# Kernel tuning notes

Measured on AMD Instinct MI355X. Metric: run time of the kernel, lower is better.

Reference implementation:

```python
import jax, jax.numpy as jnp
import numpy as np

T, BATCH, DIM = 2048, 32, 512

def setup_inputs() -> dict:
    key = jax.random.key(0)
    ks = jax.random.split(key, 9)
    s = 1.0 / np.sqrt(DIM)
    return {
        "x": jax.random.normal(ks[0], (T, BATCH, DIM), dtype=jnp.float32),
        "W_in": jax.random.uniform(ks[1], (2 * DIM, DIM), jnp.float32, -s, s),
        "b_in": jax.random.uniform(ks[2], (2 * DIM,), jnp.float32, -s, s),
        "W_out": jax.random.uniform(ks[3], (DIM, DIM), jnp.float32, -s, s),
        "b_out": jax.random.uniform(ks[4], (DIM,), jnp.float32, -s, s),
        "A": jax.random.normal(ks[5], (DIM,), dtype=jnp.float32) * 0.1,
        "B": jax.random.normal(ks[6], (DIM,), dtype=jnp.float32) * 0.1,
        "gamma": jnp.ones((DIM,), dtype=jnp.float32),
        "beta": jnp.zeros((DIM,), dtype=jnp.float32),
    }

def _layernorm(y, gamma, beta, eps=1e-5):
    mu = jnp.mean(y, axis=-1, keepdims=True)
    var = jnp.mean(jnp.square(y - mu), axis=-1, keepdims=True)
    return (y - mu) * jax.lax.rsqrt(var + eps) * gamma + beta

def reference(x, W_in, b_in, W_out, b_out, A, B, gamma, beta):
    # in_proj then chunk along last dim: z first half, g second half
    zg = jnp.einsum('tbd,ed->tbe', x, W_in) + b_in          # [T,B,2D]
    z, g = jnp.split(zg, 2, axis=-1)
    g = jax.nn.sigmoid(g)
    Bz = B * z                                              # [T,B,D]
    gA = g * A                                              # [T,B,D]

    # diagonal linear recurrence h_t = gA_t * h_{t-1} + Bz_t
    def step(prev, inp):
        ga_t, bz_t = inp
        curr = ga_t * prev + bz_t
        return curr, curr

    h0 = jnp.zeros((x.shape[1], x.shape[2]), dtype=x.dtype)
    _, h = jax.lax.scan(step, h0, (gA, Bz))                 # [T,B,D]

    out = jnp.einsum('tbd,ed->tbe', h, W_out) + b_out
    return _layernorm(x + out, gamma, beta)
```

## Files before the change

kernel.cpp:

```cpp
#include <hip/hip_runtime.h>
#include <hip/hip_bf16.h>
#include <cstdint>
#include <cstddef>

#define T_LEN 2048
#define BATCH 32
#define DIM 512
#define M_TOT (T_LEN * BATCH)
#define K_DIM DIM
#define N1 (2 * DIM)
#define NCHUNK 64
#define CLEN (T_LEN / NCHUNK)
#define BD (BATCH * DIM)
#define MT_TILES (M_TOT / 128)

typedef unsigned short ushort_t;
typedef __attribute__((ext_vector_type(8))) short short8;
typedef __attribute__((ext_vector_type(4))) float floatx4;
typedef __attribute__((ext_vector_type(4))) unsigned short ushort4v;

__device__ __forceinline__ float bf2f(ushort_t u) {
  union { unsigned int i; float f; } v;
  v.i = ((unsigned int)u) << 16;
  return v.f;
}
__device__ __forceinline__ ushort_t f2bf(float f) {
  union { float f; unsigned int i; } v;
  v.f = f;
  unsigned int x = v.i;
  return (ushort_t)((x + 0x7fffu + ((x >> 16) & 1u)) >> 16);
}

__device__ __forceinline__ void async16(const void* gp, void* lp) {
  __builtin_amdgcn_global_load_lds(
      (__attribute__((address_space(1))) void*)(void*)gp,
      (__attribute__((address_space(3))) void*)lp, 16, 0, 0);
}

__global__ __launch_bounds__(256) void cvt_f32_bf16(const float* __restrict__ in,
                                                    ushort_t* __restrict__ out,
                                                    int n4) {
  int i = blockIdx.x * 256 + threadIdx.x;
  if (i >= n4) return;
  const floatx4 v = *((const floatx4*)in + i);
  ushort4v o;
  o.x = f2bf(v.x); o.y = f2bf(v.y); o.z = f2bf(v.z); o.w = f2bf(v.w);
  *((ushort4v*)out + i) = o;
}

__global__ __launch_bounds__(256, 2) void gemm_in(
    const ushort_t* __restrict__ Ag, const ushort_t* __restrict__ Bg,
    const float* __restrict__ bias, const float* __restrict__ Avec,
    const float* __restrict__ Bvec, ushort_t* __restrict__ out0,
    ushort_t* __restrict__ out1) {
  __shared__ __align__(16) ushort_t As[128 * 64];
  __shared__ __align__(16) ushort_t Bs[128 * 64];
  const int tid = threadIdx.x;
  const int lane = tid & 63;
  const int wid = tid >> 6;
  const int wave_m = wid >> 1;
  const int wave_n = wid & 1;

  const int bid = blockIdx.x;
  const int xcd = bid & 7;
  const int slot = bid >> 3;
  const int mt = xcd * (MT_TILES / 8) + slot / 8;
  const int nt = slot % 8;
  const int m0 = mt * 128;
  const int n0 = nt * 128;

  floatx4 acc[4][4] = {};

  const int sr = tid >> 3;
  const int sc = tid & 7;

  for (int k0 = 0; k0 < K_DIM; k0 += 64) {
    __syncthreads();
#pragma unroll
    for (int i = 0; i < 4; i++) {
      const int r = i * 32 + sr;
      const int cg = sc ^ (r & 7);
      async16(Ag + (size_t)(m0 + r) * K_DIM + k0 + cg * 8,
              (char*)As + (i * 32 + wid * 8) * 128);
      async16(Bg + (size_t)(n0 + r) * K_DIM + k0 + cg * 8,
              (char*)Bs + (i * 32 + wid * 8) * 128);
    }
    __syncthreads();
#pragma unroll
    for (int kk = 0; kk < 2; kk++) {
      const int jc = kk * 4 + (lane >> 4);
      short8 af[4], bfr[4];
#pragma unroll
      for (int im = 0; im < 4; im++) {
        const int row = wave_m * 64 + im * 16 + (lane & 15);
        af[im] = *(const short8*)((const char*)As + row * 128 +
                                  ((jc ^ (row & 7)) * 16));
      }
#pragma unroll
      for (int in = 0; in < 4; in++) {
        const int row = wave_n * 64 + in * 16 + (lane & 15);
        bfr[in] = *(const short8*)((const char*)Bs + row * 128 +
                                   ((jc ^ (row & 7)) * 16));
      }
#pragma unroll
      for (int im = 0; im < 4; im++)
#pragma unroll
        for (int in = 0; in < 4; in++)
          acc[im][in] = __builtin_amdgcn_mfma_f32_16x16x32_bf16(
              af[im], bfr[in], acc[im][in], 0, 0, 0);
    }
  }

#pragma unroll
  for (int im = 0; im < 4; im++) {
#pragma unroll
    for (int in = 0; in < 4; in++) {
      const int col = n0 + wave_n * 64 + in * 16 + (lane & 15);
#pragma unroll
      for (int r = 0; r < 4; r++) {
        const int row = m0 + wave_m * 64 + im * 16 + (lane >> 4) * 4 + r;
        float val = acc[im][in][r] + bias[col];
        if (col < DIM) {
          out0[(size_t)row * DIM + col] = f2bf(Bvec[col] * val);
        } else {
          const int d = col - DIM;
          const float s = 1.f / (1.f + __expf(-val));
          out1[(size_t)row * DIM + d] = f2bf(Avec[d] * s);
        }
      }
    }
  }
}

__global__ __launch_bounds__(512, 4) void gemm_ln(
    const ushort_t* __restrict__ Ag,
    const ushort_t* __restrict__ Bg,
    const float* __restrict__ bias,
    const float* __restrict__ x,
    const float* __restrict__ gamma, const float* __restrict__ beta,
    float* __restrict__ out) {
  __shared__ __align__(16) ushort_t As[64 * 64];
  __shared__ __align__(16) ushort_t Bs[512 * 64];
  __shared__ float red[64][8][2];
  __shared__ float stat[64][2];
  const int tid = threadIdx.x;
  const int lane = tid & 63;
  const int wid = tid >> 6;
  const int m0 = blockIdx.x * 64;

  floatx4 acc[4][4] = {};
  const int sr = tid >> 3;
  const int sc = tid & 7;

  for (int k0 = 0; k0 < K_DIM; k0 += 64) {
    __syncthreads();
    {
      const int cg = sc ^ (sr & 7);
      async16(Ag + (size_t)(m0 + sr) * K_DIM + k0 + cg * 8,
              (char*)As + tid * 16);
    }
#pragma unroll
    for (int i = 0; i < 8; i++) {
      const int r = i * 64 + sr;
      const int cg = sc ^ (r & 7);
      async16(Bg + (size_t)r * K_DIM + k0 + cg * 8,
              (char*)Bs + i * 8192 + tid * 16);
    }
    __syncthreads();
#pragma unroll
    for (int kk = 0; kk < 2; kk++) {
      const int jc = kk * 4 + (lane >> 4);
      short8 af[4], bfr[4];
#pragma unroll
      for (int im = 0; im < 4; im++) {
        const int row = im * 16 + (lane & 15);
        af[im] = *(const short8*)((const char*)As + row * 128 +
                                  ((jc ^ (row & 7)) * 16));
      }
#pragma unroll
      for (int in = 0; in < 4; in++) {
        const int row = wid * 64 + in * 16 + (lane & 15);
        bfr[in] = *(const short8*)((const char*)Bs + row * 128 +
                                   ((jc ^ (row & 7)) * 16));
      }
#pragma unroll
      for (int im = 0; im < 4; im++)
#pragma unroll
        for (int in = 0; in < 4; in++)
          acc[im][in] = __builtin_amdgcn_mfma_f32_16x16x32_bf16(
              af[im], bfr[in], acc[im][in], 0, 0, 0);
    }
  }

  float bcol[4];
#pragma unroll
  for (int in = 0; in < 4; in++)
    bcol[in] = bias[wid * 64 + in * 16 + (lane & 15)];

#pragma unroll
  for (int im = 0; im < 4; im++) {
#pragma unroll
    for (int r = 0; r < 4; r++) {
      const int rowl = im * 16 + (lane >> 4) * 4 + r;
      const size_t rowg = (size_t)(m0 + rowl);
      float s = 0.f, ss = 0.f;
#pragma unroll
      for (int in = 0; in < 4; in++) {
        const int col = wid * 64 + in * 16 + (lane & 15);
        const float y = x[rowg * DIM + col] + acc[im][in][r] + bcol[in];
        s += y; ss += y * y;
      }
#pragma unroll
      for (int m = 8; m >= 1; m >>= 1) {
        s += __shfl_xor(s, m, 64);
        ss += __shfl_xor(ss, m, 64);
      }
      if ((lane & 15) == 0) {
        red[rowl][wid][0] = s;
        red[rowl][wid][1] = ss;
      }
    }
  }
  __syncthreads();
  if (tid < 64) {
    float s = 0.f, ss = 0.f;
#pragma unroll
    for (int w = 0; w < 8; w++) { s += red[tid][w][0]; ss += red[tid][w][1]; }
    const float mean = s * (1.f / DIM);
    const float var = ss * (1.f / DIM) - mean * mean;
    stat[tid][0] = mean;
    stat[tid][1] = rsqrtf(var + 1e-5f);
  }
  __syncthreads();
#pragma unroll
  for (int im = 0; im < 4; im++) {
#pragma unroll
    for (int r = 0; r < 4; r++) {
      const int rowl = im * 16 + (lane >> 4) * 4 + r;
      const size_t rowg = (size_t)(m0 + rowl);
      const float mean = stat[rowl][0], rstd = stat[rowl][1];
#pragma unroll
      for (int in = 0; in < 4; in++) {
        const int col = wid * 64 + in * 16 + (lane & 15);
        const float y = x[rowg * DIM + col] + acc[im][in][r] + bcol[in];
        out[rowg * DIM + col] = (y - mean) * rstd * gamma[col] + beta[col];
      }
    }
  }
}


__global__ __launch_bounds__(256) void scan_pass1(
    const ushort_t* __restrict__ a_arr, const ushort_t* __restrict__ bz_arr,
    float* __restrict__ pout, float* __restrict__ hout) {
  const int tid = blockIdx.x * 256 + threadIdx.x;
  const int c = tid >> 11;
  const int q = tid & 2047;
  size_t base = (size_t)(c * CLEN) * BD + q * 8;
  float h[8], p[8];
#pragma unroll
  for (int j = 0; j < 8; j++) { h[j] = 0.f; p[j] = 1.f; }
#pragma unroll 4
  for (int t = 0; t < CLEN; t++) {
    short8 av = *(const short8*)(a_arr + base + (size_t)t * BD);
    short8 bv = *(const short8*)(bz_arr + base + (size_t)t * BD);
#pragma unroll
    for (int j = 0; j < 8; j++) {
      const float a = bf2f((ushort_t)av[j]);
      h[j] = a * h[j] + bf2f((ushort_t)bv[j]);
      p[j] *= a;
    }
  }
  const size_t ci = (size_t)c * BD + q * 8;
  *(floatx4*)(pout + ci) = (floatx4){p[0], p[1], p[2], p[3]};
  *(floatx4*)(pout + ci + 4) = (floatx4){p[4], p[5], p[6], p[7]};
  *(floatx4*)(hout + ci) = (floatx4){h[0], h[1], h[2], h[3]};
  *(floatx4*)(hout + ci + 4) = (floatx4){h[4], h[5], h[6], h[7]};
}

__global__ __launch_bounds__(256) void scan_pass2(
    const float* __restrict__ p, const float* __restrict__ hend,
    float* __restrict__ carry) {
  const int q = blockIdx.x * 256 + threadIdx.x;
  float h = 0.f;
#pragma unroll 4
  for (int c = 0; c < NCHUNK; c++) {
    const size_t ci = (size_t)c * BD + q;
    const float pv = p[ci];
    const float hv = hend[ci];
    carry[ci] = h;
    h = hv + pv * h;
  }
}

__global__ __launch_bounds__(256) void scan_pass3(
    const ushort_t* __restrict__ a_arr, const ushort_t* __restrict__ bz_arr,
    const float* __restrict__ carry, ushort_t* __restrict__ h_arr) {
  const int tid = blockIdx.x * 256 + threadIdx.x;
  const int c = tid >> 11;
  const int q = tid & 2047;
  size_t base = (size_t)(c * CLEN) * BD + q * 8;
  const size_t ci = (size_t)c * BD + q * 8;
  floatx4 c0 = *(const floatx4*)(carry + ci);
  floatx4 c1 = *(const floatx4*)(carry + ci + 4);
  float h[8] = {c0.x, c0.y, c0.z, c0.w, c1.x, c1.y, c1.z, c1.w};
#pragma unroll 4
  for (int t = 0; t < CLEN; t++) {
    short8 av = *(const short8*)(a_arr + base + (size_t)t * BD);
    short8 bv = *(const short8*)(bz_arr + base + (size_t)t * BD);
    short8 o;
#pragma unroll
    for (int j = 0; j < 8; j++) {
      h[j] = bf2f((ushort_t)av[j]) * h[j] + bf2f((ushort_t)bv[j]);
      o[j] = (short)f2bf(h[j]);
    }
    *(short8*)(h_arr + base + (size_t)t * BD) = o;
  }
}

extern "C" void kernel_launch(void* const* d_in, const int* in_sizes, int n_in,
                              void* d_out, int out_size, void* d_ws,
                              size_t ws_size, hipStream_t stream) {
  const float* x = (const float*)d_in[0];
  const float* W_in = (const float*)d_in[1];
  const float* b_in = (const float*)d_in[2];
  const float* W_out = (const float*)d_in[3];
  const float* b_out = (const float*)d_in[4];
  const float* Avec = (const float*)d_in[5];
  const float* Bvec = (const float*)d_in[6];
  const float* gamma = (const float*)d_in[7];
  const float* beta = (const float*)d_in[8];
  float* out = (float*)d_out;

  char* ws = (char*)d_ws;
  const size_t SZ64 = (size_t)M_TOT * DIM * 2;
  ushort_t* xb = (ushort_t*)ws;
  ushort_t* gA = (ushort_t*)(ws + SZ64);
  ushort_t* bz = (ushort_t*)(ws + 2 * SZ64);
  ushort_t* wib = (ushort_t*)(ws + 3 * SZ64);
  ushort_t* wob = (ushort_t*)(ws + 3 * SZ64 + (size_t)N1 * K_DIM * 2);
  char* p0 = ws + 3 * SZ64 + (size_t)N1 * K_DIM * 2 + (size_t)DIM * K_DIM * 2;
  float* pc = (float*)p0;
  float* hc = (float*)(p0 + (size_t)NCHUNK * BD * 4);
  float* cc = (float*)(p0 + 2 * (size_t)NCHUNK * BD * 4);

  cvt_f32_bf16<<<(M_TOT * DIM / 4 + 255) / 256, 256, 0, stream>>>(
      x, xb, M_TOT * DIM / 4);
  cvt_f32_bf16<<<(N1 * K_DIM / 4 + 255) / 256, 256, 0, stream>>>(
      W_in, wib, N1 * K_DIM / 4);
  cvt_f32_bf16<<<(DIM * K_DIM / 4 + 255) / 256, 256, 0, stream>>>(
      W_out, wob, DIM * K_DIM / 4);

  gemm_in<<<MT_TILES * 8, 256, 0, stream>>>(
      xb, wib, b_in, Avec, Bvec, bz, gA);

  scan_pass1<<<NCHUNK * (BD / 8) / 256, 256, 0, stream>>>(gA, bz, pc, hc);
  scan_pass2<<<BD / 256, 256, 0, stream>>>(pc, hc, cc);
  scan_pass3<<<NCHUNK * (BD / 8) / 256, 256, 0, stream>>>(gA, bz, cc, xb);

  gemm_ln<<<M_TOT / 64, 512, 0, stream>>>(
      xb, wob, b_out, x, gamma, beta, out);
}
```

Measured before the change: 558.4 us.

## Stage LayerNorm output through LDS for coalesced stores; retune scan vector width

The gemm_ln epilogue now keeps the pre-norm values in the accumulators instead of re-reading x, then writes the normalized rows into a shared buffer aliased over the GEMM tiles. It stores them to global memory as coalesced 16-byte vectors in two 32-row halves. The three scan passes switch from 8 to 4 elements per thread, doubling the thread count for more parallelism, and pass2 now uses vectorized loads and stores. In exchange the kernel takes extra barriers and a larger shared allocation, which may reduce occupancy, and the scan uses narrower 8-byte loads.

```diff
diff --git a/kernel.cpp b/kernel.cpp
--- a/kernel.cpp
+++ b/kernel.cpp
@@ -139,10 +139,13 @@
     const float* __restrict__ x,
     const float* __restrict__ gamma, const float* __restrict__ beta,
     float* __restrict__ out) {
-  __shared__ __align__(16) ushort_t As[64 * 64];
-  __shared__ __align__(16) ushort_t Bs[512 * 64];
+  __shared__ __align__(16) char smem[73728];
   __shared__ float red[64][8][2];
   __shared__ float stat[64][2];
+  ushort_t* As = (ushort_t*)smem;
+  ushort_t* Bs = (ushort_t*)(smem + 8192);
+  float* ebuf = (float*)smem;
+
   const int tid = threadIdx.x;
   const int lane = tid & 63;
   const int wid = tid >> 6;
@@ -208,6 +211,7 @@
       for (int in = 0; in < 4; in++) {
         const int col = wid * 64 + in * 16 + (lane & 15);
         const float y = x[rowg * DIM + col] + acc[im][in][r] + bcol[in];
+        acc[im][in][r] = y;
         s += y; ss += y * y;
       }
 #pragma unroll
@@ -232,20 +236,35 @@
     stat[tid][1] = rsqrtf(var + 1e-5f);
   }
   __syncthreads();
-#pragma unroll
-  for (int im = 0; im < 4; im++) {
-#pragma unroll
-    for (int r = 0; r < 4; r++) {
-      const int rowl = im * 16 + (lane >> 4) * 4 + r;
-      const size_t rowg = (size_t)(m0 + rowl);
-      const float mean = stat[rowl][0], rstd = stat[rowl][1];
-#pragma unroll
-      for (int in = 0; in < 4; in++) {
-        const int col = wid * 64 + in * 16 + (lane & 15);
-        const float y = x[rowg * DIM + col] + acc[im][in][r] + bcol[in];
-        out[rowg * DIM + col] = (y - mean) * rstd * gamma[col] + beta[col];
-      }
-    }
+
+#pragma unroll
+  for (int h2 = 0; h2 < 2; h2++) {
+#pragma unroll
+    for (int imh = 0; imh < 2; imh++) {
+      const int im = h2 * 2 + imh;
+#pragma unroll
+      for (int r = 0; r < 4; r++) {
+        const int rowl = im * 16 + (lane >> 4) * 4 + r;
+        const int rloc = rowl - h2 * 32;
+        const float mean = stat[rowl][0], rstd = stat[rowl][1];
+#pragma unroll
+        for (int in = 0; in < 4; in++) {
+          const int col = wid * 64 + in * 16 + (lane & 15);
+          ebuf[rloc * 516 + col] =
+              (acc[im][in][r] - mean) * rstd * gamma[col] + beta[col];
+        }
+      }
+    }
+    __syncthreads();
+#pragma unroll
+    for (int j = 0; j < 8; j++) {
+      const int f = j * 512 + tid;
+      const int rloc = f >> 7;
+      const int coli = (f & 127) * 4;
+      const floatx4 v = *(const floatx4*)(ebuf + rloc * 516 + coli);
+      *(floatx4*)(out + (size_t)(m0 + h2 * 32 + rloc) * DIM + coli) = v;
+    }
+    __syncthreads();
   }
 }
 
@@ -254,42 +273,40 @@
     const ushort_t* __restrict__ a_arr, const ushort_t* __restrict__ bz_arr,
     float* __restrict__ pout, float* __restrict__ hout) {
   const int tid = blockIdx.x * 256 + threadIdx.x;
-  const int c = tid >> 11;
-  const int q = tid & 2047;
-  size_t base = (size_t)(c * CLEN) * BD + q * 8;
-  float h[8], p[8];
-#pragma unroll
-  for (int j = 0; j < 8; j++) { h[j] = 0.f; p[j] = 1.f; }
-#pragma unroll 4
+  const int c = tid >> 12;
+  const int q = tid & 4095;
+  size_t base = (size_t)(c * CLEN) * BD + q * 4;
+  float h0 = 0.f, h1 = 0.f, h2 = 0.f, h3 = 0.f;
+  float p0 = 1.f, p1 = 1.f, p2 = 1.f, p3 = 1.f;
+#pragma unroll 8
   for (int t = 0; t < CLEN; t++) {
-    short8 av = *(const short8*)(a_arr + base + (size_t)t * BD);
-    short8 bv = *(const short8*)(bz_arr + base + (size_t)t * BD);
-#pragma unroll
-    for (int j = 0; j < 8; j++) {
-      const float a = bf2f((ushort_t)av[j]);
-      h[j] = a * h[j] + bf2f((ushort_t)bv[j]);
-      p[j] *= a;
-    }
-  }
-  const size_t ci = (size_t)c * BD + q * 8;
-  *(floatx4*)(pout + ci) = (floatx4){p[0], p[1], p[2], p[3]};
-  *(floatx4*)(pout + ci + 4) = (floatx4){p[4], p[5], p[6], p[7]};
-  *(floatx4*)(hout + ci) = (floatx4){h[0], h[1], h[2], h[3]};
-  *(floatx4*)(hout + ci + 4) = (floatx4){h[4], h[5], h[6], h[7]};
+    ushort4v av = *(const ushort4v*)(a_arr + base + (size_t)t * BD);
+    ushort4v bv = *(const ushort4v*)(bz_arr + base + (size_t)t * BD);
+    float a0 = bf2f(av.x), a1 = bf2f(av.y), a2 = bf2f(av.z), a3 = bf2f(av.w);
+    h0 = a0 * h0 + bf2f(bv.x); p0 *= a0;
+    h1 = a1 * h1 + bf2f(bv.y); p1 *= a1;
+    h2 = a2 * h2 + bf2f(bv.z); p2 *= a2;
+    h3 = a3 * h3 + bf2f(bv.w); p3 *= a3;
+  }
+  const size_t ci = (size_t)c * BD + q * 4;
+  *(floatx4*)(pout + ci) = (floatx4){p0, p1, p2, p3};
+  *(floatx4*)(hout + ci) = (floatx4){h0, h1, h2, h3};
 }
 
 __global__ __launch_bounds__(256) void scan_pass2(
     const float* __restrict__ p, const float* __restrict__ hend,
     float* __restrict__ carry) {
   const int q = blockIdx.x * 256 + threadIdx.x;
-  float h = 0.f;
-#pragma unroll 4
+  float h0 = 0.f, h1 = 0.f, h2 = 0.f, h3 = 0.f;
   for (int c = 0; c < NCHUNK; c++) {
-    const size_t ci = (size_t)c * BD + q;
-    const float pv = p[ci];
-    const float hv = hend[ci];
-    carry[ci] = h;
-    h = hv + pv * h;
+    const size_t ci = (size_t)c * BD + q * 4;
+    floatx4 pv = *(const floatx4*)(p + ci);
+    floatx4 hv = *(const floatx4*)(hend + ci);
+    *(floatx4*)(carry + ci) = (floatx4){h0, h1, h2, h3};
+    h0 = hv.x + pv.x * h0;
+    h1 = hv.y + pv.y * h1;
+    h2 = hv.z + pv.z * h2;
+    h3 = hv.w + pv.w * h3;
   }
 }
 
@@ -297,24 +314,23 @@
     const ushort_t* __restrict__ a_arr, const ushort_t* __restrict__ bz_arr,
     const float* __restrict__ carry, ushort_t* __restrict__ h_arr) {
   const int tid = blockIdx.x * 256 + threadIdx.x;
-  const int c = tid >> 11;
-  const int q = tid & 2047;
-  size_t base = (size_t)(c * CLEN) * BD + q * 8;
-  const size_t ci = (size_t)c * BD + q * 8;
-  floatx4 c0 = *(const floatx4*)(carry + ci);
-  floatx4 c1 = *(const floatx4*)(carry + ci + 4);
-  float h[8] = {c0.x, c0.y, c0.z, c0.w, c1.x, c1.y, c1.z, c1.w};
-#pragma unroll 4
+  const int c = tid >> 12;
+  const int q = tid & 4095;
+  size_t base = (size_t)(c * CLEN) * BD + q * 4;
+  const size_t ci = (size_t)c * BD + q * 4;
+  floatx4 cv = *(const floatx4*)(carry + ci);
+  float h0 = cv.x, h1 = cv.y, h2 = cv.z, h3 = cv.w;
+#pragma unroll 8
   for (int t = 0; t < CLEN; t++) {
-    short8 av = *(const short8*)(a_arr + base + (size_t)t * BD);
-    short8 bv = *(const short8*)(bz_arr + base + (size_t)t * BD);
-    short8 o;
-#pragma unroll
-    for (int j = 0; j < 8; j++) {
-      h[j] = bf2f((ushort_t)av[j]) * h[j] + bf2f((ushort_t)bv[j]);
-      o[j] = (short)f2bf(h[j]);
-    }
-    *(short8*)(h_arr + base + (size_t)t * BD) = o;
+    ushort4v av = *(const ushort4v*)(a_arr + base + (size_t)t * BD);
+    ushort4v bv = *(const ushort4v*)(bz_arr + base + (size_t)t * BD);
+    h0 = bf2f(av.x) * h0 + bf2f(bv.x);
+    h1 = bf2f(av.y) * h1 + bf2f(bv.y);
+    h2 = bf2f(av.z) * h2 + bf2f(bv.z);
+    h3 = bf2f(av.w) * h3 + bf2f(bv.w);
+    ushort4v o;
+    o.x = f2bf(h0); o.y = f2bf(h1); o.z = f2bf(h2); o.w = f2bf(h3);
+    *(ushort4v*)(h_arr + base + (size_t)t * BD) = o;
   }
 }
 
@@ -354,9 +370,9 @@
   gemm_in<<<MT_TILES * 8, 256, 0, stream>>>(
       xb, wib, b_in, Avec, Bvec, bz, gA);
 
-  scan_pass1<<<NCHUNK * (BD / 8) / 256, 256, 0, stream>>>(gA, bz, pc, hc);
-  scan_pass2<<<BD / 256, 256, 0, stream>>>(pc, hc, cc);
-  scan_pass3<<<NCHUNK * (BD / 8) / 256, 256, 0, stream>>>(gA, bz, cc, xb);
+  scan_pass1<<<NCHUNK * (BD / 4) / 256, 256, 0, stream>>>(gA, bz, pc, hc);
+  scan_pass2<<<(BD / 4) / 256, 256, 0, stream>>>(pc, hc, cc);
+  scan_pass3<<<NCHUNK * (BD / 4) / 256, 256, 0, stream>>>(gA, bz, cc, xb);
 
   gemm_ln<<<M_TOT / 64, 512, 0, stream>>>(
       xb, wob, b_out, x, gamma, beta, out);
```

After: 508.6 us. 1.1x faster.

## Fuse x fp32-to-bf16 conversion into input GEMM and stage LN output through LDS

Applied to the files above, without the earlier changes.

Drops the separate conversion kernel for x: gemm_in now loads fp32 x tiles straight into LDS with async loads and converts them to bf16 in registers using packed cvt instructions. gemm_ln keeps the pre-norm value in the accumulators instead of re-reading x, and writes the normalized output through an LDS staging buffer so global stores become coalesced 16-byte rows. The scan pass2 unroll is also raised. The fused loads double the A-tile LDS footprint and global traffic per GEMM tile, and add conversion ALU work to the inner loop.

```diff
diff --git a/kernel.cpp b/kernel.cpp
--- a/kernel.cpp
+++ b/kernel.cpp
@@ -30,6 +30,11 @@
   unsigned int x = v.i;
   return (ushort_t)((x + 0x7fffu + ((x >> 16) & 1u)) >> 16);
 }
+__device__ __forceinline__ unsigned int cvtpk_bf16(float lo, float hi) {
+  unsigned int r;
+  asm("v_cvt_pk_bf16_f32 %0, %1, %2" : "=v"(r) : "v"(lo), "v"(hi));
+  return r;
+}
 
 __device__ __forceinline__ void async16(const void* gp, void* lp) {
   __builtin_amdgcn_global_load_lds(
@@ -49,11 +54,11 @@
 }
 
 __global__ __launch_bounds__(256, 2) void gemm_in(
-    const ushort_t* __restrict__ Ag, const ushort_t* __restrict__ Bg,
+    const float* __restrict__ Ag, const ushort_t* __restrict__ Bg,
     const float* __restrict__ bias, const float* __restrict__ Avec,
     const float* __restrict__ Bvec, ushort_t* __restrict__ out0,
     ushort_t* __restrict__ out1) {
-  __shared__ __align__(16) ushort_t As[128 * 64];
+  __shared__ __align__(16) float Asf[128 * 64];
   __shared__ __align__(16) ushort_t Bs[128 * 64];
   const int tid = threadIdx.x;
   const int lane = tid & 63;
@@ -73,15 +78,22 @@
 
   const int sr = tid >> 3;
   const int sc = tid & 7;
+  const int sr16 = tid >> 4;
+  const int sc16 = tid & 15;
 
   for (int k0 = 0; k0 < K_DIM; k0 += 64) {
     __syncthreads();
+#pragma unroll
+    for (int i = 0; i < 8; i++) {
+      const int r = i * 16 + sr16;
+      const int cg = sc16 ^ (r & 15);
+      async16(Ag + (size_t)(m0 + r) * K_DIM + k0 + cg * 4,
+              (char*)Asf + i * 4096 + tid * 16);
+    }
 #pragma unroll
     for (int i = 0; i < 4; i++) {
       const int r = i * 32 + sr;
       const int cg = sc ^ (r & 7);
-      async16(Ag + (size_t)(m0 + r) * K_DIM + k0 + cg * 8,
-              (char*)As + (i * 32 + wid * 8) * 128);
       async16(Bg + (size_t)(n0 + r) * K_DIM + k0 + cg * 8,
               (char*)Bs + (i * 32 + wid * 8) * 128);
     }
@@ -93,8 +105,17 @@
 #pragma unroll
       for (int im = 0; im < 4; im++) {
         const int row = wave_m * 64 + im * 16 + (lane & 15);
-        af[im] = *(const short8*)((const char*)As + row * 128 +
-                                  ((jc ^ (row & 7)) * 16));
+        const int rx = row & 15;
+        const floatx4 a0 = *(const floatx4*)(
+            (const char*)Asf + row * 256 + (((2 * jc) ^ rx) << 4));
+        const floatx4 a1 = *(const floatx4*)(
+            (const char*)Asf + row * 256 + (((2 * jc + 1) ^ rx) << 4));
+        union { unsigned int u[4]; short8 s; } pk;
+        pk.u[0] = cvtpk_bf16(a0.x, a0.y);
+        pk.u[1] = cvtpk_bf16(a0.z, a0.w);
+        pk.u[2] = cvtpk_bf16(a1.x, a1.y);
+        pk.u[3] = cvtpk_bf16(a1.z, a1.w);
+        af[im] = pk.s;
       }
 #pragma unroll
       for (int in = 0; in < 4; in++) {
@@ -139,10 +160,13 @@
     const float* __restrict__ x,
     const float* __restrict__ gamma, const float* __restrict__ beta,
     float* __restrict__ out) {
-  __shared__ __align__(16) ushort_t As[64 * 64];
-  __shared__ __align__(16) ushort_t Bs[512 * 64];
+  __shared__ __align__(16) char smem[73728];
   __shared__ float red[64][8][2];
   __shared__ float stat[64][2];
+  ushort_t* As = (ushort_t*)smem;
+  ushort_t* Bs = (ushort_t*)(smem + 8192);
+  float* ebuf = (float*)smem;
+
   const int tid = threadIdx.x;
   const int lane = tid & 63;
   const int wid = tid >> 6;
@@ -208,6 +232,7 @@
       for (int in = 0; in < 4; in++) {
         const int col = wid * 64 + in * 16 + (lane & 15);
         const float y = x[rowg * DIM + col] + acc[im][in][r] + bcol[in];
+        acc[im][in][r] = y;
         s += y; ss += y * y;
       }
 #pragma unroll
@@ -232,20 +257,35 @@
     stat[tid][1] = rsqrtf(var + 1e-5f);
   }
   __syncthreads();
-#pragma unroll
-  for (int im = 0; im < 4; im++) {
-#pragma unroll
-    for (int r = 0; r < 4; r++) {
-      const int rowl = im * 16 + (lane >> 4) * 4 + r;
-      const size_t rowg = (size_t)(m0 + rowl);
-      const float mean = stat[rowl][0], rstd = stat[rowl][1];
-#pragma unroll
-      for (int in = 0; in < 4; in++) {
-        const int col = wid * 64 + in * 16 + (lane & 15);
-        const float y = x[rowg * DIM + col] + acc[im][in][r] + bcol[in];
-        out[rowg * DIM + col] = (y - mean) * rstd * gamma[col] + beta[col];
-      }
-    }
+
+#pragma unroll
+  for (int h2 = 0; h2 < 2; h2++) {
+#pragma unroll
+    for (int imh = 0; imh < 2; imh++) {
+      const int im = h2 * 2 + imh;
+#pragma unroll
+      for (int r = 0; r < 4; r++) {
+        const int rowl = im * 16 + (lane >> 4) * 4 + r;
+        const int rloc = rowl - h2 * 32;
+        const float mean = stat[rowl][0], rstd = stat[rowl][1];
+#pragma unroll
+        for (int in = 0; in < 4; in++) {
+          const int col = wid * 64 + in * 16 + (lane & 15);
+          ebuf[rloc * 516 + col] =
+              (acc[im][in][r] - mean) * rstd * gamma[col] + beta[col];
+        }
+      }
+    }
+    __syncthreads();
+#pragma unroll
+    for (int j = 0; j < 8; j++) {
+      const int f = j * 512 + tid;
+      const int rloc = f >> 7;
+      const int coli = (f & 127) * 4;
+      const floatx4 v = *(const floatx4*)(ebuf + rloc * 516 + coli);
+      *(floatx4*)(out + (size_t)(m0 + h2 * 32 + rloc) * DIM + coli) = v;
+    }
+    __syncthreads();
   }
 }
 
@@ -283,7 +323,7 @@
     float* __restrict__ carry) {
   const int q = blockIdx.x * 256 + threadIdx.x;
   float h = 0.f;
-#pragma unroll 4
+#pragma unroll 8
   for (int c = 0; c < NCHUNK; c++) {
     const size_t ci = (size_t)c * BD + q;
     const float pv = p[ci];
@@ -334,7 +374,7 @@
 
   char* ws = (char*)d_ws;
   const size_t SZ64 = (size_t)M_TOT * DIM * 2;
-  ushort_t* xb = (ushort_t*)ws;
+  ushort_t* hb = (ushort_t*)ws;
   ushort_t* gA = (ushort_t*)(ws + SZ64);
   ushort_t* bz = (ushort_t*)(ws + 2 * SZ64);
   ushort_t* wib = (ushort_t*)(ws + 3 * SZ64);
@@ -344,20 +384,18 @@
   float* hc = (float*)(p0 + (size_t)NCHUNK * BD * 4);
   float* cc = (float*)(p0 + 2 * (size_t)NCHUNK * BD * 4);
 
-  cvt_f32_bf16<<<(M_TOT * DIM / 4 + 255) / 256, 256, 0, stream>>>(
-      x, xb, M_TOT * DIM / 4);
   cvt_f32_bf16<<<(N1 * K_DIM / 4 + 255) / 256, 256, 0, stream>>>(
       W_in, wib, N1 * K_DIM / 4);
   cvt_f32_bf16<<<(DIM * K_DIM / 4 + 255) / 256, 256, 0, stream>>>(
       W_out, wob, DIM * K_DIM / 4);
 
   gemm_in<<<MT_TILES * 8, 256, 0, stream>>>(
-      xb, wib, b_in, Avec, Bvec, bz, gA);
+      x, wib, b_in, Avec, Bvec, bz, gA);
 
   scan_pass1<<<NCHUNK * (BD / 8) / 256, 256, 0, stream>>>(gA, bz, pc, hc);
   scan_pass2<<<BD / 256, 256, 0, stream>>>(pc, hc, cc);
-  scan_pass3<<<NCHUNK * (BD / 8) / 256, 256, 0, stream>>>(gA, bz, cc, xb);
+  scan_pass3<<<NCHUNK * (BD / 8) / 256, 256, 0, stream>>>(gA, bz, cc, hb);
 
   gemm_ln<<<M_TOT / 64, 512, 0, stream>>>(
-      xb, wob, b_out, x, gamma, beta, out);
-}
+      hb, wob, b_out, x, gamma, beta, out);
+}
```

New measurement: 547.1 us. -2.0%, faster.
